# Kernel optimization log

Measured on AMD Instinct MI355X. Metric: run time of the kernel, lower is better.

## Reference

```python
import jax, jax.numpy as jnp
from jax import lax
import numpy as np

B, W, M, F = 8, 20, 512, 16
H = 128          # n_hidden
HALF = 64        # half_hid
K = 10           # conv out channels
LONG_K = W // 2  # dilated conv kernel


def setup_inputs() -> dict:
    key = jax.random.key(0)
    ks = jax.random.split(key, 24)
    s = 0.1  # weight scale (xavier-ish)
    return {
        "X": jax.random.normal(ks[0], (B, W, M, F), jnp.float32),
        "Y": jax.random.uniform(ks[1], (B, M), jnp.float32),
        "adj": jax.random.uniform(ks[2], (M, M), jnp.float32),
        "V": jax.random.normal(ks[3], (HALF,), jnp.float32) * s,
        "bv": jax.random.normal(ks[4], (1,), jnp.float32) * s,
        "W1": jax.random.normal(ks[5], (HALF, H), jnp.float32) * s,
        "b1": jax.random.normal(ks[6], (HALF,), jnp.float32) * s,
        "W2": jax.random.normal(ks[7], (HALF, H), jnp.float32) * s,
        "Wb": jax.random.normal(ks[8], (M, M), jnp.float32) * s,
        "wb": jax.random.normal(ks[9], (1,), jnp.float32) * s,
        "conv_w": jax.random.normal(ks[10], (K, F, W), jnp.float32) * s,
        "conv_b": jax.random.normal(ks[11], (K,), jnp.float32) * s,
        "convl_w": jax.random.normal(ks[12], (K, F, LONG_K), jnp.float32) * s,
        "convl_b": jax.random.normal(ks[13], (K,), jnp.float32) * s,
        "gru_Wih": jax.random.normal(ks[14], (3 * H, F), jnp.float32) * s,
        "gru_Whh": jax.random.normal(ks[15], (3 * H, H), jnp.float32) * s,
        "gru_bih": jax.random.normal(ks[16], (3 * H,), jnp.float32) * s,
        "gru_bhh": jax.random.normal(ks[17], (3 * H,), jnp.float32) * s,
        "gc1_W": jax.random.normal(ks[18], (3 * K, H), jnp.float32) * s,
        "gc1_b": jax.random.normal(ks[19], (H,), jnp.float32) * s,
        "gc2_W": jax.random.normal(ks[20], (H, K), jnp.float32) * s,
        "gc2_b": jax.random.normal(ks[21], (K,), jnp.float32) * s,
        "out_W": jax.random.normal(ks[22], (1, H + K), jnp.float32) * s,
        "out_b": jax.random.normal(ks[23], (1,), jnp.float32) * s,
    }


def _gru_last(xseq, Wih, Whh, bih, bhh):
    # xseq: (N, T, F) -> last hidden (N, H), PyTorch GRU gate order r,z,n
    n_hid = Whh.shape[1]
    def step(h, x_t):
        gx = x_t @ Wih.T + bih
        gh = h @ Whh.T + bhh
        xr, xz, xn = jnp.split(gx, 3, axis=-1)
        hr, hz, hn = jnp.split(gh, 3, axis=-1)
        r = jax.nn.sigmoid(xr + hr)
        z = jax.nn.sigmoid(xz + hz)
        n = jnp.tanh(xn + r * hn)
        return (1.0 - z) * n + z * h, None
    h0 = jnp.zeros((xseq.shape[0], n_hid), xseq.dtype)
    hT, _ = lax.scan(step, h0, jnp.moveaxis(xseq, 1, 0))
    return hT


def _forward(X, Y, adj, V, bv, W1, b1, W2, Wb, wb, conv_w, conv_b, convl_w,
             convl_b, gru_Wih, gru_Whh, gru_bih, gru_bhh, gc1_W, gc1_b,
             gc2_W, gc2_b, out_W, out_b):
    b, w, m, f = X.shape
    # ---- temporal branch: GRU per node ----
    x = jnp.transpose(X, (0, 2, 1, 3)).reshape(b * m, w, f)
    last_hid = _gru_last(x, gru_Wih, gru_Whh, gru_bih, gru_bhh).reshape(b, m, -1)
    out_temporal = last_hid
    # ---- attention-style adaptive adjacency ----
    # hid_rpt_m[b,i,j]=last_hid[b,j]; hid_rpt_w[b,i,j]=last_hid[b,i]
    p1 = jnp.einsum('bjh,kh->bjk', last_hid, W1)  # pairs with column index j
    p2 = jnp.einsum('bih,kh->bik', last_hid, W2)  # pairs with row index i
    pre = p1[:, None, :, :] + p2[:, :, None, :] + b1  # (b,m,m,half)
    a_mx = jnp.einsum('bijk,k->bij', jax.nn.elu(pre), V) + bv[0]
    # F.normalize(p=2, dim=1)
    nrm = jnp.sqrt(jnp.sum(a_mx * a_mx, axis=1, keepdims=True))
    a_mx = a_mx / jnp.maximum(nrm, 1e-12)
    # ---- per-node conv1d (vectorized over nodes) ----
    Xc = jnp.transpose(X, (0, 2, 3, 1)).reshape(b * m, f, w)  # (bm, f, w)
    dn = ('NCH', 'OIH', 'NCH')
    r = lax.conv_general_dilated(Xc, conv_w, (1,), 'VALID', dimension_numbers=dn)
    r = r + conv_b[None, :, None]                      # (bm, K, 1)
    rl = lax.conv_general_dilated(Xc, convl_w, (1,), 'VALID',
                                  rhs_dilation=(2,), dimension_numbers=dn)
    rl = rl + convl_b[None, :, None]                   # (bm, K, long_out)
    r_cat = jnp.concatenate([r, rl], axis=-1)          # (bm, K, 1+long_out)
    r_l = jax.nn.relu(r_cat.reshape(b, m, -1))         # (b, m, (1+long_out)*K)
    # ---- gate learned adjacency with fixed adjacency ----
    c = jax.nn.sigmoid(jnp.einsum('bij,jk->bik', a_mx, Wb) + wb[0])
    A = adj[None] * c + a_mx * (1.0 - c)               # (b,m,m)
    # ---- graph convolutions: out = A @ (x @ W) + b ----
    h1 = jax.nn.relu(jnp.einsum('bij,bjh->bih', A, r_l @ gc1_W) + gc1_b)
    out_spatial = jax.nn.relu(jnp.einsum('bij,bjh->bih', A, h1 @ gc2_W) + gc2_b)
    # ---- readout ----
    out = jnp.concatenate([out_spatial, out_temporal], axis=-1)
    out = (out @ out_W.T + out_b).squeeze(-1)          # (b, m)
    y = out.reshape(-1)
    Yf = Y.reshape(-1)
    # BCE with logits: softplus(y) - Y*y, averaged
    loss = jnp.mean(jax.nn.softplus(y) - Yf * y)
    return loss, jax.nn.sigmoid(y)


def reference(X, Y, adj, V, bv, W1, b1, W2, Wb, wb, conv_w, conv_b, convl_w,
              convl_b, gru_Wih, gru_Whh, gru_bih, gru_bhh, gc1_W, gc1_b,
              gc2_W, gc2_b, out_W, out_b):
    return _forward(X, Y, adj, V, bv, W1, b1, W2, Wb, wb, conv_w, conv_b,
                    convl_w, convl_b, gru_Wih, gru_Whh, gru_bih, gru_bhh,
                    gc1_W, gc1_b, gc2_W, gc2_b, out_W, out_b)
```

## Files before the change

### kernel.cpp

```cpp
#include <hip/hip_runtime.h>
#include <math.h>

#define Bn 8
#define Wn 20
#define Mn 512
#define Fn 16
#define Hn 128
#define HALFn 64
#define Kn 10

typedef __attribute__((ext_vector_type(8))) short short8;
typedef __attribute__((ext_vector_type(4))) float f32x4;
typedef unsigned short ushort_t;

__device__ __forceinline__ float sigmoidf_(float x) {
  return 1.0f / (1.0f + __expf(-x));
}
__device__ __forceinline__ float tanhf_(float x) {
  float xx = fminf(fmaxf(x, -15.f), 15.f);
  float e = __expf(2.f * xx);
  return (e - 1.f) / (e + 1.f);
}
__device__ __forceinline__ float reluf_(float x) { return fmaxf(x, 0.f); }
__device__ __forceinline__ float eluf_(float x) {
  return (x > 0.f) ? x : (__expf(x) - 1.f);
}
__device__ __forceinline__ ushort_t bf16_rne(float v) {
  unsigned u = __float_as_uint(v);
  u += 0x7FFFu + ((u >> 16) & 1u);
  return (ushort_t)(u >> 16);
}
__device__ __forceinline__ float bf16_to_f(ushort_t b) {
  return __uint_as_float(((unsigned)b) << 16);
}

__global__ __launch_bounds__(256) void pack_kernel(
    const float* __restrict__ Whh, const float* __restrict__ Wih,
    const float* __restrict__ Wb, ushort_t* __restrict__ Bpack,
    ushort_t* __restrict__ WbT_hi, ushort_t* __restrict__ WbT_lo,
    float* __restrict__ ssq, float* __restrict__ d_out) {
  int tid = threadIdx.x;
  if (blockIdx.x < 240) {
    int idx = blockIdx.x * 256 + tid;
    if (idx < 4096) ssq[idx] = 0.f;
    if (idx == 0) d_out[0] = 0.f;
    if (idx >= 24 * 5 * 512) return;
    int j = idx & 7;
    int lane = (idx >> 3) & 63;
    int ks = (idx >> 9) % 5;
    int nt = idx / (5 * 512);
    int k = ks * 32 + (lane >> 4) * 8 + j;
    int g = (nt & 7) * 16 + (nt >> 3) * 128 + (lane & 15);
    float val = 0.f;
    if (k < 128) val = Whh[g * 128 + k];
    else if (k < 144) val = Wih[g * 16 + (k - 128)];
    ushort_t hb = bf16_rne(val);
    float lo = val - bf16_to_f(hb);
    Bpack[(((long)nt * 5 + ks) * 2 + 0) * 512 + lane * 8 + j] = hb;
    Bpack[(((long)nt * 5 + ks) * 2 + 1) * 512 + lane * 8 + j] = bf16_rne(lo);
  } else {
    int t = blockIdx.x - 240;
    int k0 = (t >> 3) * 64, j0 = (t & 7) * 64;
    __shared__ float wt[64][65];
    for (int idx = tid; idx < 4096; idx += 256) {
      int r = idx >> 6, c = idx & 63;
      wt[r][c] = Wb[(long)(k0 + r) * 512 + j0 + c];
    }
    __syncthreads();
    for (int idx = tid; idx < 4096; idx += 256) {
      int r = idx >> 6, c = idx & 63;
      float v = wt[c][r];
      ushort_t hb = bf16_rne(v);
      WbT_hi[(long)(j0 + r) * 512 + k0 + c] = hb;
      WbT_lo[(long)(j0 + r) * 512 + k0 + c] = bf16_rne(v - bf16_to_f(hb));
    }
  }
}

#define LDK 168
#define HSZ (16 * LDK)
__global__ __launch_bounds__(512, 1) void gru_kernel(
    const float* __restrict__ X, const ushort_t* __restrict__ Bpack,
    const float* __restrict__ bih, const float* __restrict__ bhh,
    const float* __restrict__ W1, const float* __restrict__ W2,
    const float* __restrict__ b1, float* __restrict__ last_hid,
    float* __restrict__ p1, float* __restrict__ p2) {
  const int tid = threadIdx.x;
  const int wave = tid >> 6;
  const int lane = tid & 63;
  const int quad = lane >> 4;
  const int jl = lane & 15;
  const int j0 = wave * 16;
  const int blk = blockIdx.x;
  const int b = blk >> 5;
  const int m0 = (blk & 31) * 16;

  __shared__ __align__(16) ushort_t smem_hs[4 * HSZ];

  short8 frR[5][2], frZ[5][2], frN[4][2], frXN[2];
#pragma unroll
  for (int ks = 0; ks < 5; ++ks) {
#pragma unroll
    for (int p = 0; p < 2; ++p) {
      frR[ks][p] = *(const short8*)&Bpack[(((long)(wave) * 5 + ks) * 2 + p) * 512 + lane * 8];
      frZ[ks][p] = *(const short8*)&Bpack[(((long)(8 + wave) * 5 + ks) * 2 + p) * 512 + lane * 8];
    }
  }
#pragma unroll
  for (int ks = 0; ks < 4; ++ks) {
#pragma unroll
    for (int p = 0; p < 2; ++p)
      frN[ks][p] = *(const short8*)&Bpack[(((long)(16 + wave) * 5 + ks) * 2 + p) * 512 + lane * 8];
  }
#pragma unroll
  for (int p = 0; p < 2; ++p)
    frXN[p] = *(const short8*)&Bpack[(((long)(16 + wave) * 5 + 4) * 2 + p) * 512 + lane * 8];

  const float cr  = bih[j0 + jl] + bhh[j0 + jl];
  const float cz  = bih[128 + j0 + jl] + bhh[128 + j0 + jl];
  const float cnx = bih[256 + j0 + jl];
  const float cnh = bhh[256 + j0 + jl];

  for (int i = tid; i < 4 * HSZ; i += 512) smem_hs[i] = 0;

  const float* Xb = X + (long)b * (Wn * Mn * Fn) + (long)m0 * Fn;
  float x0 = 0.f;
  if (tid < 256) x0 = Xb[tid];
// ... 42 lines not shown
#pragma unroll
    for (int reg = 0; reg < 4; ++reg) {
      float r = sigmoidf_(aR[0][reg] + aR[1][reg] + cr);
      float z = sigmoidf_(aZ[0][reg] + aZ[1][reg] + cz);
      float n = tanhf_(aXN[reg] + cnx + r * (aHN[0][reg] + aHN[1][reg] + cnh));
      float h = (1.f - z) * n + z * hp[reg];
      hp[reg] = h;
      int s = quad * 4 + reg;
      ushort_t hb = bf16_rne(h);
      smem_hs[hiN + s * LDK + j0 + jl] = hb;
      smem_hs[loN + s * LDK + j0 + jl] = bf16_rne(h - bf16_to_f(hb));
    }
    if (tid < 256 && t < Wn - 1) {
      int s = tid >> 4, f = tid & 15;
      ushort_t hb = bf16_rne(xpre);
      smem_hs[hiN + s * LDK + 128 + f] = hb;
      smem_hs[loN + s * LDK + 128 + f] = bf16_rne(xpre - bf16_to_f(hb));
    }
    __syncthreads();
  }

  float* hs_f = (float*)smem_hs;
#pragma unroll
  for (int reg = 0; reg < 4; ++reg) {
    int s = quad * 4 + reg;
    float h = hp[reg];
    last_hid[(long)(blk * 16 + s) * Hn + j0 + jl] = h;
    hs_f[s * 132 + j0 + jl] = h;
  }
  __syncthreads();
  {
    int k = tid & 63;
    int part = (tid >> 6) & 1;
    int sg = tid >> 7;
    const float* Wp = part ? W2 : W1;
    float a[4];
    float init = part ? 0.f : b1[k];
    a[0] = a[1] = a[2] = a[3] = init;
    for (int h = 0; h < 128; h += 4) {
      float4 w = *(const float4*)&Wp[k * 128 + h];
#pragma unroll
      for (int rr = 0; rr < 4; ++rr) {
        float4 q = *(const float4*)&hs_f[(sg * 4 + rr) * 132 + h];
        a[rr] += q.x * w.x + q.y * w.y + q.z * w.z + q.w * w.w;
      }
    }
    float* outp = part ? p2 : p1;
#pragma unroll
    for (int rr = 0; rr < 4; ++rr)
      outp[(long)(blk * 16 + sg * 4 + rr) * 64 + k] = a[rr];
  }
}

__global__ __launch_bounds__(128) void conv_t1_kernel(
    const float* __restrict__ X, const float* __restrict__ conv_w,
    const float* __restrict__ conv_b, const float* __restrict__ convl_w,
    const float* __restrict__ convl_b, const float* __restrict__ gc1_W,
    ushort_t* __restrict__ t1T_hi, ushort_t* __restrict__ t1T_lo) {
  int tid = threadIdx.x;
  int n0 = blockIdx.x * 8;
  int b = n0 >> 9, m0 = n0 & 511;
  __shared__ float xs[8][16][20];
  __shared__ float cw[3200];
  __shared__ float clw[1600];
  __shared__ float rs[8][32];
  for (int idx = tid; idx < 3200; idx += 128) cw[idx] = conv_w[idx];
  for (int idx = tid; idx < 1600; idx += 128) clw[idx] = convl_w[idx];
  for (int w = 0; w < 20; ++w)
    xs[tid >> 4][tid & 15][w] = X[((long)(b * 20 + w) * 512 + m0) * 16 + tid];
  __syncthreads();
  if (tid < 80) {
    int s = tid / 10, k = tid % 10;
    float a0 = conv_b[k];
    float l0 = convl_b[k], l1 = convl_b[k];
    for (int f = 0; f < 16; ++f) {
#pragma unroll
      for (int w = 0; w < 20; ++w) a0 = fmaf(xs[s][f][w], cw[k * 320 + f * 20 + w], a0);
#pragma unroll
      for (int q = 0; q < 10; ++q) {
        float wv = clw[k * 160 + f * 10 + q];
        l0 = fmaf(xs[s][f][2 * q], wv, l0);
        l1 = fmaf(xs[s][f][2 * q + 1], wv, l1);
      }
    }
    rs[s][k * 3 + 0] = reluf_(a0);
    rs[s][k * 3 + 1] = reluf_(l0);
    rs[s][k * 3 + 2] = reluf_(l1);
  }
  __syncthreads();
  float w[30];
#pragma unroll
  for (int q = 0; q < 30; ++q) w[q] = gc1_W[q * 128 + tid];
  long base = ((long)b * 128 + tid) * 512 + m0;
#pragma unroll
  for (int s = 0; s < 8; ++s) {
    float a = 0.f;
#pragma unroll
    for (int q = 0; q < 30; ++q) a = fmaf(rs[s][q], w[q], a);
    ushort_t hb = bf16_rne(a);
    t1T_hi[base + s] = hb;
    t1T_lo[base + s] = bf16_rne(a - bf16_to_f(hb));
  }
}

__global__ __launch_bounds__(256) void amx_kernel(
    const float* __restrict__ p1, const float* __restrict__ p2,
    const float* __restrict__ V, const float* __restrict__ bv,
    float* __restrict__ amx, float* __restrict__ ssq) {
  int tid = threadIdx.x;
  int j0 = blockIdx.x * 32, i0 = blockIdx.y * 32, bz = blockIdx.z;
  __shared__ float p1s[32][68];
  __shared__ float p2s[32][68];
  __shared__ float Vs[64];
  __shared__ float cred[16][33];
  if (tid < 64) Vs[tid] = V[tid];
  {
    int rr = tid >> 3, c0 = (tid & 7) * 8;
    *(float4*)&p1s[rr][c0]     = *(const float4*)&p1[(long)(bz * 512 + j0 + rr) * 64 + c0];
    *(float4*)&p1s[rr][c0 + 4] = *(const float4*)&p1[(long)(bz * 512 + j0 + rr) * 64 + c0 + 4];
    *(float4*)&p2s[rr][c0]     = *(const float4*)&p2[(long)(bz * 512 + i0 + rr) * 64 + c0];
    *(float4*)&p2s[rr][c0 + 4] = *(const float4*)&p2[(long)(bz * 512 + i0 + rr) * 64 + c0 + 4];
  }
  __syncthreads();
  int r0 = tid >> 4, c0 = tid & 15;
  float acc[2][2] = {{0.f, 0.f}, {0.f, 0.f}};
  for (int k = 0; k < 64; ++k) {
    float vj0 = p1s[c0][k], vj1 = p1s[c0 + 16][k];
    float vi0 = p2s[r0][k], vi1 = p2s[r0 + 16][k];
    float vk = Vs[k];
    acc[0][0] = fmaf(eluf_(vj0 + vi0), vk, acc[0][0]);
    acc[0][1] = fmaf(eluf_(vj1 + vi0), vk, acc[0][1]);
    acc[1][0] = fmaf(eluf_(vj0 + vi1), vk, acc[1][0]);
    acc[1][1] = fmaf(eluf_(vj1 + vi1), vk, acc[1][1]);
  }
  float bvv = bv[0];
  float s2[2] = {0.f, 0.f};
#pragma unroll
  for (int a = 0; a < 2; ++a)
#pragma unroll
    for (int c = 0; c < 2; ++c) {
      float v = acc[a][c] + bvv;
      amx[((long)(bz * 512 + i0 + r0 + a * 16)) * 512 + j0 + c0 + c * 16] = v;
      s2[c] += v * v;
    }
  cred[r0][c0] = s2[0];
  cred[r0][c0 + 16] = s2[1];
  __syncthreads();
  if (tid < 32) {
    float s = 0.f;
#pragma unroll
    for (int p = 0; p < 16; ++p) s += cred[p][tid];
    atomicAdd(&ssq[bz * 512 + j0 + tid], s);
  }
}

#define CPK 40
__global__ __launch_bounds__(256, 2) void gemm_cA(
    const float* __restrict__ amx, const ushort_t* __restrict__ WbT_hi,
    const ushort_t* __restrict__ WbT_lo, const float* __restrict__ adj,
    const float* __restrict__ wb, const float* __restrict__ ssq,
    float* __restrict__ A) {
  const int bz = blockIdx.z;
  const int i0 = blockIdx.y * 64;
  const int j0 = blockIdx.x * 64;
  const int tid = threadIdx.x;
  const int wave = tid >> 6;
  const int lane = tid & 63;
  const int quad = lane >> 4, jl = lane & 15;
  const int wm = (wave & 1) * 32, wn = (wave >> 1) * 32;

  __shared__ __align__(16) ushort_t Ahi[64][CPK];
  __shared__ __align__(16) ushort_t Alo[64][CPK];
  __shared__ __align__(16) ushort_t Bhi[64][CPK];
  __shared__ __align__(16) ushort_t Blo[64][CPK];
  __shared__ float rs_s[512];

  const float* Abase = amx + (long)bz * 262144;
  const float* sb = ssq + bz * 512;
  for (int i = tid; i < 512; i += 256)
    rs_s[i] = 1.f / fmaxf(sqrtf(sb[i]), 1e-12f);

  f32x4 acc[2][2];
#pragma unroll
  for (int a = 0; a < 2; ++a)
#pragma unroll
    for (int c = 0; c < 2; ++c) acc[a][c] = (f32x4){0.f, 0.f, 0.f, 0.f};

  for (int kk0 = 0; kk0 < 512; kk0 += 32) {
    __syncthreads();
#pragma unroll
    for (int l = 0; l < 2; ++l) {
      int e = l * 1024 + tid * 4;
      int r = e >> 5, kq = e & 31;
      float4 v = *(const float4*)&Abase[(long)(i0 + r) * 512 + kk0 + kq];
      float4 sc = *(const float4*)&rs_s[kk0 + kq];
      float vv[4] = {v.x * sc.x, v.y * sc.y, v.z * sc.z, v.w * sc.w};
#pragma unroll
      for (int q = 0; q < 4; ++q) {
        ushort_t hb = bf16_rne(vv[q]);
        Ahi[r][kq + q] = hb;
        Alo[r][kq + q] = bf16_rne(vv[q] - bf16_to_f(hb));
      }
    }
    {
      int r = tid >> 2, kc = (tid & 3) * 8;
      *(uint4*)&Bhi[r][kc] = *(const uint4*)&WbT_hi[(long)(j0 + r) * 512 + kk0 + kc];
      *(uint4*)&Blo[r][kc] = *(const uint4*)&WbT_lo[(long)(j0 + r) * 512 + kk0 + kc];
    }
    __syncthreads();
    short8 ah[2], al[2], bh[2], bl[2];
#pragma unroll
    for (int tm = 0; tm < 2; ++tm) {
      ah[tm] = *(const short8*)&Ahi[wm + tm * 16 + jl][quad * 8];
      al[tm] = *(const short8*)&Alo[wm + tm * 16 + jl][quad * 8];
    }
#pragma unroll
    for (int tn = 0; tn < 2; ++tn) {
      bh[tn] = *(const short8*)&Bhi[wn + tn * 16 + jl][quad * 8];
      bl[tn] = *(const short8*)&Blo[wn + tn * 16 + jl][quad * 8];
    }
#pragma unroll
    for (int tm = 0; tm < 2; ++tm)
#pragma unroll
      for (int tn = 0; tn < 2; ++tn) {
        acc[tm][tn] = __builtin_amdgcn_mfma_f32_16x16x32_bf16(ah[tm], bh[tn], acc[tm][tn], 0, 0, 0);
        acc[tm][tn] = __builtin_amdgcn_mfma_f32_16x16x32_bf16(ah[tm], bl[tn], acc[tm][tn], 0, 0, 0);
        acc[tm][tn] = __builtin_amdgcn_mfma_f32_16x16x32_bf16(al[tm], bh[tn], acc[tm][tn], 0, 0, 0);
      }
  }

  const float wbv = wb[0];
#pragma unroll
  for (int tn = 0; tn < 2; ++tn) {
    int j = j0 + wn + tn * 16 + jl;
    float sj = rs_s[j];
#pragma unroll
    for (int tm = 0; tm < 2; ++tm) {
#pragma unroll
      for (int reg = 0; reg < 4; ++reg) {
        int i = i0 + wm + tm * 16 + quad * 4 + reg;
        long ofs = (long)bz * 262144 + (long)i * 512 + j;
        float c = sigmoidf_(acc[tm][tn][reg] + wbv);
        float am = Abase[(long)i * 512 + j] * sj;
        float ad = adj[(long)i * 512 + j];
        A[ofs] = ad * c + am * (1.f - c);
      }
    }
  }
}

__global__ __launch_bounds__(512, 1) void gemm_h1t2(
    const float* __restrict__ A, const ushort_t* __restrict__ t1T_hi,
    const ushort_t* __restrict__ t1T_lo, const float* __restrict__ gc1_b,
    const float* __restrict__ gc2_W, float* __restrict__ t2) {
  const int bz = blockIdx.y;
  const int i0 = blockIdx.x * 16;
  const int tid = threadIdx.x;
  const int wave = tid >> 6;
  const int lane = tid & 63;
  const int quad = lane >> 4, jl = lane & 15;

  __shared__ __align__(16) ushort_t Ahi[16][CPK];
  __shared__ __align__(16) ushort_t Alo[16][CPK];
  __shared__ __align__(16) ushort_t Bhi[128][CPK];
  __shared__ __align__(16) ushort_t Blo[128][CPK];
  __shared__ float h1s[16][132];
  __shared__ float gw[1280];

  const float* Ab = A + (long)bz * 262144;
  for (int idx = tid; idx < 1280; idx += 512) gw[idx] = gc2_W[idx];

  f32x4 acc = {0.f, 0.f, 0.f, 0.f};

  for (int kk0 = 0; kk0 < 512; kk0 += 32) {
    __syncthreads();
    {
      int r = tid >> 5, kq = tid & 31;
      float v = Ab[(long)(i0 + r) * 512 + kk0 + kq];
      ushort_t hb = bf16_rne(v);
      Ahi[r][kq] = hb;
      Alo[r][kq] = bf16_rne(v - bf16_to_f(hb));
    }
    {
      int r = tid >> 2, kc = (tid & 3) * 8;
      *(uint4*)&Bhi[r][kc] = *(const uint4*)&t1T_hi[((long)bz * 128 + r) * 512 + kk0 + kc];
      *(uint4*)&Blo[r][kc] = *(const uint4*)&t1T_lo[((long)bz * 128 + r) * 512 + kk0 + kc];
    }
    __syncthreads();
    short8 ah = *(const short8*)&Ahi[jl][quad * 8];
    short8 al = *(const short8*)&Alo[jl][quad * 8];
    short8 bh = *(const short8*)&Bhi[wave * 16 + jl][quad * 8];
    short8 bl = *(const short8*)&Blo[wave * 16 + jl][quad * 8];
    acc = __builtin_amdgcn_mfma_f32_16x16x32_bf16(ah, bh, acc, 0, 0, 0);
    acc = __builtin_amdgcn_mfma_f32_16x16x32_bf16(ah, bl, acc, 0, 0, 0);
    acc = __builtin_amdgcn_mfma_f32_16x16x32_bf16(al, bh, acc, 0, 0, 0);
  }
  __syncthreads();
  {
    int n = wave * 16 + jl;
    float bb = gc1_b[n];
#pragma unroll
    for (int reg = 0; reg < 4; ++reg) {
      int r = quad * 4 + reg;
      h1s[r][n] = reluf_(acc[reg] + bb);
    }
  }
  __syncthreads();
  if (tid < 160) {
    int r = tid / 10, c = tid % 10;
    float a = 0.f;
#pragma unroll 4
    for (int k = 0; k < 128; ++k) a = fmaf(h1s[r][k], gw[k * 10 + c], a);
    t2[((long)bz * 512 + i0 + r) * 10 + c] = a;
  }
}

__global__ __launch_bounds__(256) void spat_readout(
    const float* __restrict__ A, const float* __restrict__ t2,
    const float* __restrict__ gc2_b, const float* __restrict__ last_hid,
    const float* __restrict__ out_W, const float* __restrict__ out_b,
    const float* __restrict__ Y, float* __restrict__ d_out) {
  int tid = threadIdx.x;
  int bz = blockIdx.y;
  int i0 = blockIdx.x * 8;
  __shared__ float t2s[5120];
  __shared__ float wS[138];
  __shared__ float osps[8][12];
  for (int idx = tid; idx < 5120; idx += 256) t2s[idx] = t2[(long)bz * 5120 + idx];
  for (int idx = tid; idx < 138; idx += 256) wS[idx] = out_W[idx];
  __syncthreads();
  int r = tid >> 5, sk = tid & 31;
  const float* Arow = A + (long)bz * 262144 + (long)(i0 + r) * 512;
  float acc[10] = {0, 0, 0, 0, 0, 0, 0, 0, 0, 0};
  for (int k = sk; k < 512; k += 32) {
    float av = Arow[k];
    const float* tp = &t2s[k * 10];
#pragma unroll
    for (int c = 0; c < 10; ++c) acc[c] = fmaf(av, tp[c], acc[c]);
  }
#pragma unroll
  for (int off = 16; off; off >>= 1)
#pragma unroll
    for (int c = 0; c < 10; ++c) acc[c] += __shfl_xor(acc[c], off);
  if (sk == 0) {
#pragma unroll
    for (int c = 0; c < 10; ++c) osps[r][c] = reluf_(acc[c] + gc2_b[c]);
  }
  __syncthreads();
  float l = 0.f;
  if (tid < 8) {
    int gid = bz * 512 + i0 + tid;
    float y = out_b[0];
#pragma unroll
    for (int k = 0; k < 10; ++k) y = fmaf(osps[tid][k], wS[k], y);
    const float* hp = &last_hid[(long)gid * 128];
    for (int h = 0; h < 128; h += 4) {
      float4 hv = *(const float4*)&hp[h];
      y = fmaf(hv.x, wS[10 + h + 0], y);
      y = fmaf(hv.y, wS[10 + h + 1], y);
      y = fmaf(hv.z, wS[10 + h + 2], y);
      y = fmaf(hv.w, wS[10 + h + 3], y);
    }
    d_out[1 + gid] = sigmoidf_(y);
    l = fmaxf(y, 0.f) + log1pf(__expf(-fabsf(y))) - Y[gid] * y;
  }
  if (tid < 64) {
#pragma unroll
    for (int off = 4; off; off >>= 1) l += __shfl_down(l, off);
    if (tid == 0) atomicAdd(d_out, l * (1.0f / 4096.f));
  }
}

extern "C" void kernel_launch(void* const* d_in, const int* in_sizes, int n_in,
                              void* d_out, int out_size, void* d_ws, size_t ws_size,
                              hipStream_t stream) {
  const float* X       = (const float*)d_in[0];
  const float* Y       = (const float*)d_in[1];
  const float* adj     = (const float*)d_in[2];
  const float* V       = (const float*)d_in[3];
  const float* bv      = (const float*)d_in[4];
  const float* W1      = (const float*)d_in[5];
  const float* b1      = (const float*)d_in[6];
  const float* W2      = (const float*)d_in[7];
  const float* Wb      = (const float*)d_in[8];
  const float* wb      = (const float*)d_in[9];
  const float* conv_w  = (const float*)d_in[10];
  const float* conv_b  = (const float*)d_in[11];
  const float* convl_w = (const float*)d_in[12];
  const float* convl_b = (const float*)d_in[13];
  const float* gWih    = (const float*)d_in[14];
  const float* gWhh    = (const float*)d_in[15];
  const float* gbih    = (const float*)d_in[16];
  const float* gbhh    = (const float*)d_in[17];
  const float* gc1_W   = (const float*)d_in[18];
  const float* gc1_b   = (const float*)d_in[19];
  const float* gc2_W   = (const float*)d_in[20];
  const float* gc2_b   = (const float*)d_in[21];
  const float* out_W   = (const float*)d_in[22];
  const float* out_b   = (const float*)d_in[23];
  float* out = (float*)d_out;

  float* ws = (float*)d_ws;
  float* lhid  = ws; ws += 524288;
  float* p1    = ws; ws += 262144;
  float* p2    = ws; ws += 262144;
  float* amx   = ws; ws += 2097152;
  float* ssq   = ws; ws += 4096;
  float* Abuf  = ws; ws += 2097152;
  float* t2    = ws; ws += 40960;
  float* Bpkf  = ws; ws += 122880;
  float* WbTf  = ws; ws += 262144;
  float* t1Tf  = ws; ws += 524288;
  if (ws_size < (size_t)(ws - (float*)d_ws) * sizeof(float)) return;
  ushort_t* Bpack  = (ushort_t*)Bpkf;
  ushort_t* WbT_hi = (ushort_t*)WbTf;
  ushort_t* WbT_lo = WbT_hi + 262144;
  ushort_t* t1T_hi = (ushort_t*)t1Tf;
  ushort_t* t1T_lo = t1T_hi + 524288;

  pack_kernel<<<304, 256, 0, stream>>>(gWhh, gWih, Wb, Bpack, WbT_hi, WbT_lo,
                                       ssq, out);
  gru_kernel<<<256, 512, 0, stream>>>(X, Bpack, gbih, gbhh, W1, W2, b1,
                                      lhid, p1, p2);
  conv_t1_kernel<<<512, 128, 0, stream>>>(X, conv_w, conv_b, convl_w, convl_b,
                                          gc1_W, t1T_hi, t1T_lo);
  amx_kernel<<<dim3(16, 16, 8), 256, 0, stream>>>(p1, p2, V, bv, amx, ssq);
  gemm_cA<<<dim3(8, 8, 8), 256, 0, stream>>>(amx, WbT_hi, WbT_lo, adj, wb,
                                             ssq, Abuf);
  gemm_h1t2<<<dim3(32, 8), 512, 0, stream>>>(Abuf, t1T_hi, t1T_lo, gc1_b,
                                             gc2_W, t2);
  spat_readout<<<dim3(64, 8), 256, 0, stream>>>(Abuf, t2, gc2_b, lhid,
                                                out_W, out_b, Y, out);
}
```

Measured before the change: 256.1 us.

## Fuse pack with conv and merge tail stages into one cooperative kernel

Merges the weight-packing and conv/t1 kernels into one prep kernel, and folds the amx, gate GEMM, graph-conv GEMM and readout kernels into a single cooperative kernel separated by grid-wide syncs. The amx stage now has each block own a column strip, so column norms are computed locally with no atomics and no ssq zeroing. The aim is to remove launch gaps and inter-kernel drain between many small stages. In exchange it adds grid.sync overhead and fixes the tail to 512 blocks of 256 threads, which needs two resident blocks per CU; the h1/t2 stage uses only half the grid.

```diff
diff --git a/kernel.cpp b/kernel.cpp
--- a/kernel.cpp
+++ b/kernel.cpp
@@ -1,13 +1,14 @@
 #include <hip/hip_runtime.h>
+#include <hip/hip_cooperative_groups.h>
 #include <math.h>
+
+namespace cg = cooperative_groups;
 
 #define Bn 8
 #define Wn 20
 #define Mn 512
 #define Fn 16
 #define Hn 128
-#define HALFn 64
-#define Kn 10
 
 typedef __attribute__((ext_vector_type(8))) short short8;
 typedef __attribute__((ext_vector_type(4))) float f32x4;
@@ -34,45 +35,99 @@
   return __uint_as_float(((unsigned)b) << 16);
 }
 
-__global__ __launch_bounds__(256) void pack_kernel(
+__global__ __launch_bounds__(256) void prep_kernel(
+    const float* __restrict__ X, const float* __restrict__ conv_w,
+    const float* __restrict__ conv_b, const float* __restrict__ convl_w,
+    const float* __restrict__ convl_b, const float* __restrict__ gc1_W,
     const float* __restrict__ Whh, const float* __restrict__ Wih,
     const float* __restrict__ Wb, ushort_t* __restrict__ Bpack,
     ushort_t* __restrict__ WbT_hi, ushort_t* __restrict__ WbT_lo,
-    float* __restrict__ ssq, float* __restrict__ d_out) {
-  int tid = threadIdx.x;
-  if (blockIdx.x < 240) {
-    int idx = blockIdx.x * 256 + tid;
-    if (idx < 4096) ssq[idx] = 0.f;
-    if (idx == 0) d_out[0] = 0.f;
-    if (idx >= 24 * 5 * 512) return;
-    int j = idx & 7;
-    int lane = (idx >> 3) & 63;
-    int ks = (idx >> 9) % 5;
-    int nt = idx / (5 * 512);
+    ushort_t* __restrict__ t1T_hi, ushort_t* __restrict__ t1T_lo,
+    float* __restrict__ d_out) {
+  int tid = threadIdx.x, blk = blockIdx.x;
+  __shared__ __align__(16) char sm[30720];
+  float* xs  = (float*)sm;
+  float* cw  = (float*)(sm + 10240);
+  float* clw = (float*)(sm + 23040);
+  float* rs  = (float*)(sm + 29440);
+
+  int gidx = blk * 256 + tid;
+  if (gidx == 0) d_out[0] = 0.f;
+  if (gidx < 24 * 5 * 512) {
+    int j = gidx & 7;
+    int lane = (gidx >> 3) & 63;
+    int ks = (gidx >> 9) % 5;
+    int nt = gidx / (5 * 512);
     int k = ks * 32 + (lane >> 4) * 8 + j;
     int g = (nt & 7) * 16 + (nt >> 3) * 128 + (lane & 15);
     float val = 0.f;
     if (k < 128) val = Whh[g * 128 + k];
     else if (k < 144) val = Wih[g * 16 + (k - 128)];
     ushort_t hb = bf16_rne(val);
-    float lo = val - bf16_to_f(hb);
     Bpack[(((long)nt * 5 + ks) * 2 + 0) * 512 + lane * 8 + j] = hb;
-    Bpack[(((long)nt * 5 + ks) * 2 + 1) * 512 + lane * 8 + j] = bf16_rne(lo);
-  } else {
-    int t = blockIdx.x - 240;
-    int k0 = (t >> 3) * 64, j0 = (t & 7) * 64;
-    __shared__ float wt[64][65];
+    Bpack[(((long)nt * 5 + ks) * 2 + 1) * 512 + lane * 8 + j] =
+        bf16_rne(val - bf16_to_f(hb));
+  }
+
+  int n0 = blk * 8, b = n0 >> 9, m0 = n0 & 511;
+  for (int idx = tid; idx < 3200; idx += 256) cw[idx] = conv_w[idx];
+  for (int idx = tid; idx < 1600; idx += 256) clw[idx] = convl_w[idx];
+  if (tid < 128) {
+    for (int w = 0; w < 20; ++w)
+      xs[tid * 20 + w] = X[((long)(b * 20 + w) * 512 + m0) * 16 + tid];
+  }
+  __syncthreads();
+  if (tid < 80) {
+    int s = tid / 10, k = tid % 10;
+    float a0 = conv_b[k];
+    float l0 = convl_b[k], l1 = convl_b[k];
+    for (int f = 0; f < 16; ++f) {
+      const float* xp = &xs[(s * 16 + f) * 20];
+#pragma unroll
+      for (int w = 0; w < 20; ++w) a0 = fmaf(xp[w], cw[k * 320 + f * 20 + w], a0);
+#pragma unroll
+      for (int q = 0; q < 10; ++q) {
+        float wv = clw[k * 160 + f * 10 + q];
+        l0 = fmaf(xp[2 * q], wv, l0);
+        l1 = fmaf(xp[2 * q + 1], wv, l1);
+      }
+    }
+    rs[s * 32 + k * 3 + 0] = reluf_(a0);
+    rs[s * 32 + k * 3 + 1] = reluf_(l0);
+    rs[s * 32 + k * 3 + 2] = reluf_(l1);
+  }
+  __syncthreads();
+  if (tid < 128) {
+    float w[30];
+#pragma unroll
+    for (int q = 0; q < 30; ++q) w[q] = gc1_W[q * 128 + tid];
+    long base = ((long)b * 128 + tid) * 512 + m0;
+#pragma unroll
+    for (int s = 0; s < 8; ++s) {
+      float a = 0.f;
+#pragma unroll
+      for (int q = 0; q < 30; ++q) a = fmaf(rs[s * 32 + q], w[q], a);
+      ushort_t hb = bf16_rne(a);
+      t1T_hi[base + s] = hb;
+      t1T_lo[base + s] = bf16_rne(a - bf16_to_f(hb));
+    }
+  }
+
+  if (blk < 64) {
+    __syncthreads();
+    float* wt = (float*)sm;
+    int k0 = (blk >> 3) * 64, j0w = (blk & 7) * 64;
     for (int idx = tid; idx < 4096; idx += 256) {
       int r = idx >> 6, c = idx & 63;
-      wt[r][c] = Wb[(long)(k0 + r) * 512 + j0 + c];
+      wt[r * 65 + c] = Wb[(long)(k0 + r) * 512 + j0w + c];
     }
     __syncthreads();
     for (int idx = tid; idx < 4096; idx += 256) {
       int r = idx >> 6, c = idx & 63;
-      float v = wt[c][r];
+      float v = wt[c * 65 + r];
       ushort_t hb = bf16_rne(v);
-      WbT_hi[(long)(j0 + r) * 512 + k0 + c] = hb;
-      WbT_lo[(long)(j0 + r) * 512 + k0 + c] = bf16_rne(v - bf16_to_f(hb));
+      WbT_hi[(long)(j0w + r) * 512 + k0 + c] = hb;
+      WbT_lo[(long)(j0w + r) * 512 + k0 + c] = bf16_rne(v - bf16_to_f(hb));
     }
   }
 }
@@ -221,322 +276,264 @@
   }
 }
 
-__global__ __launch_bounds__(128) void conv_t1_kernel(
-    const float* __restrict__ X, const float* __restrict__ conv_w,
-    const float* __restrict__ conv_b, const float* __restrict__ convl_w,
-    const float* __restrict__ convl_b, const float* __restrict__ gc1_W,
-    ushort_t* __restrict__ t1T_hi, ushort_t* __restrict__ t1T_lo) {
-  int tid = threadIdx.x;
-  int n0 = blockIdx.x * 8;
-  int b = n0 >> 9, m0 = n0 & 511;
-  __shared__ float xs[8][16][20];
-  __shared__ float cw[3200];
-  __shared__ float clw[1600];
-  __shared__ float rs[8][32];
-  for (int idx = tid; idx < 3200; idx += 128) cw[idx] = conv_w[idx];
-  for (int idx = tid; idx < 1600; idx += 128) clw[idx] = convl_w[idx];
-  for (int w = 0; w < 20; ++w)
-    xs[tid >> 4][tid & 15][w] = X[((long)(b * 20 + w) * 512 + m0) * 16 + tid];
-  __syncthreads();
-  if (tid < 80) {
-    int s = tid / 10, k = tid % 10;
-    float a0 = conv_b[k];
-    float l0 = convl_b[k], l1 = convl_b[k];
-    for (int f = 0; f < 16; ++f) {
-#pragma unroll
-      for (int w = 0; w < 20; ++w) a0 = fmaf(xs[s][f][w], cw[k * 320 + f * 20 + w], a0);
-#pragma unroll
-      for (int q = 0; q < 10; ++q) {
-        float wv = clw[k * 160 + f * 10 + q];
-        l0 = fmaf(xs[s][f][2 * q], wv, l0);
-        l1 = fmaf(xs[s][f][2 * q + 1], wv, l1);
-      }
-    }
-    rs[s][k * 3 + 0] = reluf_(a0);
-    rs[s][k * 3 + 1] = reluf_(l0);
-    rs[s][k * 3 + 2] = reluf_(l1);
-  }
-  __syncthreads();
-  float w[30];
-#pragma unroll
-  for (int q = 0; q < 30; ++q) w[q] = gc1_W[q * 128 + tid];
-  long base = ((long)b * 128 + tid) * 512 + m0;
-#pragma unroll
-  for (int s = 0; s < 8; ++s) {
-    float a = 0.f;
-#pragma unroll
-    for (int q = 0; q < 30; ++q) a = fmaf(rs[s][q], w[q], a);
-    ushort_t hb = bf16_rne(a);
-    t1T_hi[base + s] = hb;
-    t1T_lo[base + s] = bf16_rne(a - bf16_to_f(hb));
-  }
-}
-
-__global__ __launch_bounds__(256) void amx_kernel(
-    const float* __restrict__ p1, const float* __restrict__ p2,
-    const float* __restrict__ V, const float* __restrict__ bv,
-    float* __restrict__ amx, float* __restrict__ ssq) {
-  int tid = threadIdx.x;
-  int j0 = blockIdx.x * 32, i0 = blockIdx.y * 32, bz = blockIdx.z;
-  __shared__ float p1s[32][68];
-  __shared__ float p2s[32][68];
-  __shared__ float Vs[64];
-  __shared__ float cred[16][33];
-  if (tid < 64) Vs[tid] = V[tid];
-  {
-    int rr = tid >> 3, c0 = (tid & 7) * 8;
-    *(float4*)&p1s[rr][c0]     = *(const float4*)&p1[(long)(bz * 512 + j0 + rr) * 64 + c0];
-    *(float4*)&p1s[rr][c0 + 4] = *(const float4*)&p1[(long)(bz * 512 + j0 + rr) * 64 + c0 + 4];
-    *(float4*)&p2s[rr][c0]     = *(const float4*)&p2[(long)(bz * 512 + i0 + rr) * 64 + c0];
-    *(float4*)&p2s[rr][c0 + 4] = *(const float4*)&p2[(long)(bz * 512 + i0 + rr) * 64 + c0 + 4];
-  }
-  __syncthreads();
-  int r0 = tid >> 4, c0 = tid & 15;
-  float acc[2][2] = {{0.f, 0.f}, {0.f, 0.f}};
-  for (int k = 0; k < 64; ++k) {
-    float vj0 = p1s[c0][k], vj1 = p1s[c0 + 16][k];
-    float vi0 = p2s[r0][k], vi1 = p2s[r0 + 16][k];
-    float vk = Vs[k];
-    acc[0][0] = fmaf(eluf_(vj0 + vi0), vk, acc[0][0]);
-    acc[0][1] = fmaf(eluf_(vj1 + vi0), vk, acc[0][1]);
-    acc[1][0] = fmaf(eluf_(vj0 + vi1), vk, acc[1][0]);
-    acc[1][1] = fmaf(eluf_(vj1 + vi1), vk, acc[1][1]);
-  }
-  float bvv = bv[0];
-  float s2[2] = {0.f, 0.f};
-#pragma unroll
-  for (int a = 0; a < 2; ++a)
-#pragma unroll
-    for (int c = 0; c < 2; ++c) {
-      float v = acc[a][c] + bvv;
-      amx[((long)(bz * 512 + i0 + r0 + a * 16)) * 512 + j0 + c0 + c * 16] = v;
-      s2[c] += v * v;
-    }
-  cred[r0][c0] = s2[0];
-  cred[r0][c0 + 16] = s2[1];
-  __syncthreads();
-  if (tid < 32) {
-    float s = 0.f;
-#pragma unroll
-    for (int p = 0; p < 16; ++p) s += cred[p][tid];
-    atomicAdd(&ssq[bz * 512 + j0 + tid], s);
-  }
-}
+struct TArgs {
+  const float *p1, *p2, *V, *bv, *adj, *wb, *gc1_b, *gc2_W, *gc2_b;
+  const float *last_hid, *out_W, *out_b, *Y;
+  const ushort_t *WbT_hi, *WbT_lo, *t1T_hi, *t1T_lo;
+  float *amx, *scl, *A, *t2, *out;
+};
 
 #define CPK 40
-__global__ __launch_bounds__(256, 2) void gemm_cA(
-    const float* __restrict__ amx, const ushort_t* __restrict__ WbT_hi,
-    const ushort_t* __restrict__ WbT_lo, const float* __restrict__ adj,
-    const float* __restrict__ wb, const float* __restrict__ ssq,
-    float* __restrict__ A) {
-  const int bz = blockIdx.z;
-  const int i0 = blockIdx.y * 64;
-  const int j0 = blockIdx.x * 64;
+__global__ __launch_bounds__(256, 2) void tail_kernel(TArgs a) {
+  cg::grid_group grid = cg::this_grid();
   const int tid = threadIdx.x;
+  const int blk = blockIdx.x;
   const int wave = tid >> 6;
   const int lane = tid & 63;
   const int quad = lane >> 4, jl = lane & 15;
-  const int wm = (wave & 1) * 32, wn = (wave >> 1) * 32;
-
-  __shared__ __align__(16) ushort_t Ahi[64][CPK];
-  __shared__ __align__(16) ushort_t Alo[64][CPK];
-  __shared__ __align__(16) ushort_t Bhi[64][CPK];
-  __shared__ __align__(16) ushort_t Blo[64][CPK];
-  __shared__ float rs_s[512];
-
-  const float* Abase = amx + (long)bz * 262144;
-  const float* sb = ssq + bz * 512;
-  for (int i = tid; i < 512; i += 256)
-    rs_s[i] = 1.f / fmaxf(sqrtf(sb[i]), 1e-12f);
-
-  f32x4 acc[2][2];
-#pragma unroll
-  for (int a = 0; a < 2; ++a)
-#pragma unroll
-    for (int c = 0; c < 2; ++c) acc[a][c] = (f32x4){0.f, 0.f, 0.f, 0.f};
-
-  for (int kk0 = 0; kk0 < 512; kk0 += 32) {
-    __syncthreads();
-#pragma unroll
-    for (int l = 0; l < 2; ++l) {
-      int e = l * 1024 + tid * 4;
-      int r = e >> 5, kq = e & 31;
-      float4 v = *(const float4*)&Abase[(long)(i0 + r) * 512 + kk0 + kq];
-      float4 sc = *(const float4*)&rs_s[kk0 + kq];
-      float vv[4] = {v.x * sc.x, v.y * sc.y, v.z * sc.z, v.w * sc.w};
-#pragma unroll
-      for (int q = 0; q < 4; ++q) {
-        ushort_t hb = bf16_rne(vv[q]);
-        Ahi[r][kq + q] = hb;
-        Alo[r][kq + q] = bf16_rne(vv[q] - bf16_to_f(hb));
-      }
-    }
-    {
-      int r = tid >> 2, kc = (tid & 3) * 8;
-      *(uint4*)&Bhi[r][kc] = *(const uint4*)&WbT_hi[(long)(j0 + r) * 512 + kk0 + kc];
-      *(uint4*)&Blo[r][kc] = *(const uint4*)&WbT_lo[(long)(j0 + r) * 512 + kk0 + kc];
-    }
-    __syncthreads();
-    short8 ah[2], al[2], bh[2], bl[2];
-#pragma unroll
-    for (int tm = 0; tm < 2; ++tm) {
-      ah[tm] = *(const short8*)&Ahi[wm + tm * 16 + jl][quad * 8];
-      al[tm] = *(const short8*)&Alo[wm + tm * 16 + jl][quad * 8];
-    }
+  __shared__ __align__(16) char sm[36864];
+
+  {
+    float* Vs   = (float*)sm;
+    float* p1s  = (float*)(sm + 256);
+    float* p2s  = (float*)(sm + 2432);
+    float* sred = (float*)(sm + 11136);
+    int j0 = (blk & 63) * 8, bz = blk >> 6;
+    if (tid < 64) Vs[tid] = a.V[tid];
+    for (int idx = tid; idx < 512; idx += 256) {
+      int r = idx >> 6, k = idx & 63;
+      p1s[r * 68 + k] = a.p1[(long)(bz * 512 + j0 + r) * 64 + k];
+    }
+    float bvv = a.bv[0];
+    int r = tid >> 3, c = tid & 7;
+    float ss = 0.f;
+    for (int it = 0; it < 16; ++it) {
+      int i0 = it * 32;
+      __syncthreads();
+      for (int idx = tid; idx < 2048; idx += 256) {
+        int rr = idx >> 6, k = idx & 63;
+        p2s[rr * 68 + k] = a.p2[(long)(bz * 512 + i0 + rr) * 64 + k];
+      }
+      __syncthreads();
+      float acc = 0.f;
+#pragma unroll 4
+      for (int k = 0; k < 64; ++k)
+        acc = fmaf(eluf_(p1s[c * 68 + k] + p2s[r * 68 + k]), Vs[k], acc);
+      float v = acc + bvv;
+      a.amx[((long)(bz * 512 + i0 + r)) * 512 + j0 + c] = v;
+      ss += v * v;
+    }
+    sred[r * 8 + c] = ss;
+    __syncthreads();
+    if (tid < 8) {
+      float s = 0.f;
+#pragma unroll
+      for (int p = 0; p < 32; ++p) s += sred[p * 8 + tid];
+      a.scl[bz * 512 + j0 + tid] = 1.f / fmaxf(sqrtf(s), 1e-12f);
+    }
+  }
+  __threadfence();
+  grid.sync();
+
+  {
+    ushort_t* Ahi = (ushort_t*)sm;
+    ushort_t* Alo = (ushort_t*)(sm + 5120);
+    ushort_t* Bhi = (ushort_t*)(sm + 10240);
+    ushort_t* Blo = (ushort_t*)(sm + 15360);
+    float*    rsS = (float*)(sm + 20480);
+    int bx = blk & 7, by = (blk >> 3) & 7, bz = blk >> 6;
+    int i0 = by * 64, j0 = bx * 64;
+    const int wm = (wave & 1) * 32, wn = (wave >> 1) * 32;
+    const float* Abase = a.amx + (long)bz * 262144;
+    for (int i = tid; i < 512; i += 256) rsS[i] = a.scl[bz * 512 + i];
+
+    f32x4 acc[2][2];
+#pragma unroll
+    for (int q = 0; q < 2; ++q)
+#pragma unroll
+      for (int w = 0; w < 2; ++w) acc[q][w] = (f32x4){0.f, 0.f, 0.f, 0.f};
+
+    for (int kk0 = 0; kk0 < 512; kk0 += 32) {
+      __syncthreads();
+#pragma unroll
+      for (int l = 0; l < 2; ++l) {
+        int e = l * 1024 + tid * 4;
+        int r = e >> 5, kq = e & 31;
+        float4 v = *(const float4*)&Abase[(long)(i0 + r) * 512 + kk0 + kq];
+        float4 sc = *(const float4*)&rsS[kk0 + kq];
+        float vv[4] = {v.x * sc.x, v.y * sc.y, v.z * sc.z, v.w * sc.w};
+#pragma unroll
+        for (int q = 0; q < 4; ++q) {
+          ushort_t hb = bf16_rne(vv[q]);
+          Ahi[r * CPK + kq + q] = hb;
+          Alo[r * CPK + kq + q] = bf16_rne(vv[q] - bf16_to_f(hb));
+        }
+      }
+      {
+        int r = tid >> 2, kc = (tid & 3) * 8;
+        *(uint4*)&Bhi[r * CPK + kc] = *(const uint4*)&a.WbT_hi[(long)(j0 + r) * 512 + kk0 + kc];
+        *(uint4*)&Blo[r * CPK + kc] = *(const uint4*)&a.WbT_lo[(long)(j0 + r) * 512 + kk0 + kc];
+      }
+      __syncthreads();
+      short8 ah[2], al[2], bh[2], bl[2];
+#pragma unroll
+      for (int tm = 0; tm < 2; ++tm) {
+        ah[tm] = *(const short8*)&Ahi[(wm + tm * 16 + jl) * CPK + quad * 8];
+        al[tm] = *(const short8*)&Alo[(wm + tm * 16 + jl) * CPK + quad * 8];
+      }
+#pragma unroll
+      for (int tn = 0; tn < 2; ++tn) {
+        bh[tn] = *(const short8*)&Bhi[(wn + tn * 16 + jl) * CPK + quad * 8];
+        bl[tn] = *(const short8*)&Blo[(wn + tn * 16 + jl) * CPK + quad * 8];
+      }
+#pragma unroll
+      for (int tm = 0; tm < 2; ++tm)
+#pragma unroll
+        for (int tn = 0; tn < 2; ++tn) {
+          acc[tm][tn] = __builtin_amdgcn_mfma_f32_16x16x32_bf16(ah[tm], bh[tn], acc[tm][tn], 0, 0, 0);
+          acc[tm][tn] = __builtin_amdgcn_mfma_f32_16x16x32_bf16(ah[tm], bl[tn], acc[tm][tn], 0, 0, 0);
+          acc[tm][tn] = __builtin_amdgcn_mfma_f32_16x16x32_bf16(al[tm], bh[tn], acc[tm][tn], 0, 0, 0);
+        }
+    }
+    const float wbv = a.wb[0];
 #pragma unroll
     for (int tn = 0; tn < 2; ++tn) {
-      bh[tn] = *(const short8*)&Bhi[wn + tn * 16 + jl][quad * 8];
-      bl[tn] = *(const short8*)&Blo[wn + tn * 16 + jl][quad * 8];
-    }
-#pragma unroll
-    for (int tm = 0; tm < 2; ++tm)
+      int j = j0 + wn + tn * 16 + jl;
+      float sj = rsS[j];
+#pragma unroll
+      for (int tm = 0; tm < 2; ++tm) {
+#pragma unroll
+        for (int reg = 0; reg < 4; ++reg) {
+          int i = i0 + wm + tm * 16 + quad * 4 + reg;
+          long ofs = (long)bz * 262144 + (long)i * 512 + j;
+          float c = sigmoidf_(acc[tm][tn][reg] + wbv);
+          float am = Abase[(long)i * 512 + j] * sj;
+          float ad = a.adj[(long)i * 512 + j];
+          a.A[ofs] = ad * c + am * (1.f - c);
+        }
+      }
+    }
+  }
+  __threadfence();
+  grid.sync();
+
+  if (blk < 256) {
+    ushort_t* Ahi = (ushort_t*)sm;
+    ushort_t* Alo = (ushort_t*)(sm + 1280);
+    ushort_t* Bhi = (ushort_t*)(sm + 2560);
+    ushort_t* Blo = (ushort_t*)(sm + 12800);
+    float*    h1s = (float*)(sm + 23040);
+    float*    gw  = (float*)(sm + 31488);
+    int ib = blk & 31, bz = blk >> 5;
+    int i0 = ib * 16;
+    const float* Ab = a.A + (long)bz * 262144;
+    for (int idx = tid; idx < 1280; idx += 256) gw[idx] = a.gc2_W[idx];
+
+    f32x4 acc[2];
+    acc[0] = acc[1] = (f32x4){0.f, 0.f, 0.f, 0.f};
+    for (int kk0 = 0; kk0 < 512; kk0 += 32) {
+      __syncthreads();
+      {
+        int e = tid * 2;
+        int r = e >> 5, kq = e & 31;
+        float2 v = *(const float2*)&Ab[(long)(i0 + r) * 512 + kk0 + kq];
+        ushort_t hb0 = bf16_rne(v.x);
+        Ahi[r * CPK + kq] = hb0;
+        Alo[r * CPK + kq] = bf16_rne(v.x - bf16_to_f(hb0));
+        ushort_t hb1 = bf16_rne(v.y);
+        Ahi[r * CPK + kq + 1] = hb1;
+        Alo[r * CPK + kq + 1] = bf16_rne(v.y - bf16_to_f(hb1));
+      }
+#pragma unroll
+      for (int l = 0; l < 2; ++l) {
+        int e = l * 2048 + tid * 8;
+        int r = e >> 5, kc = e & 31;
+        *(uint4*)&Bhi[r * CPK + kc] = *(const uint4*)&a.t1T_hi[((long)bz * 128 + r) * 512 + kk0 + kc];
+        *(uint4*)&Blo[r * CPK + kc] = *(const uint4*)&a.t1T_lo[((long)bz * 128 + r) * 512 + kk0 + kc];
+      }
+      __syncthreads();
+      short8 ah = *(const short8*)&Ahi[jl * CPK + quad * 8];
+      short8 al = *(const short8*)&Alo[jl * CPK + quad * 8];
 #pragma unroll
       for (int tn = 0; tn < 2; ++tn) {
-        acc[tm][tn] = __builtin_amdgcn_mfma_f32_16x16x32_bf16(ah[tm], bh[tn], acc[tm][tn], 0, 0, 0);
-        acc[tm][tn] = __builtin_amdgcn_mfma_f32_16x16x32_bf16(ah[tm], bl[tn], acc[tm][tn], 0, 0, 0);
-        acc[tm][tn] = __builtin_amdgcn_mfma_f32_16x16x32_bf16(al[tm], bh[tn], acc[tm][tn], 0, 0, 0);
-      }
-  }
-
-  const float wbv = wb[0];
-#pragma unroll
-  for (int tn = 0; tn < 2; ++tn) {
-    int j = j0 + wn + tn * 16 + jl;
-    float sj = rs_s[j];
-#pragma unroll
-    for (int tm = 0; tm < 2; ++tm) {
+        short8 bh = *(const short8*)&Bhi[(wave * 32 + tn * 16 + jl) * CPK + quad * 8];
+        short8 bl = *(const short8*)&Blo[(wave * 32 + tn * 16 + jl) * CPK + quad * 8];
+        acc[tn] = __builtin_amdgcn_mfma_f32_16x16x32_bf16(ah, bh, acc[tn], 0, 0, 0);
+        acc[tn] = __builtin_amdgcn_mfma_f32_16x16x32_bf16(ah, bl, acc[tn], 0, 0, 0);
+        acc[tn] = __builtin_amdgcn_mfma_f32_16x16x32_bf16(al, bh, acc[tn], 0, 0, 0);
+      }
+    }
+    __syncthreads();
+#pragma unroll
+    for (int tn = 0; tn < 2; ++tn) {
+      int n = wave * 32 + tn * 16 + jl;
+      float bb = a.gc1_b[n];
 #pragma unroll
       for (int reg = 0; reg < 4; ++reg) {
-        int i = i0 + wm + tm * 16 + quad * 4 + reg;
-        long ofs = (long)bz * 262144 + (long)i * 512 + j;
-        float c = sigmoidf_(acc[tm][tn][reg] + wbv);
-        float am = Abase[(long)i * 512 + j] * sj;
-        float ad = adj[(long)i * 512 + j];
-        A[ofs] = ad * c + am * (1.f - c);
-      }
-    }
-  }
-}
-
-__global__ __launch_bounds__(512, 1) void gemm_h1t2(
-    const float* __restrict__ A, const ushort_t* __restrict__ t1T_hi,
-    const ushort_t* __restrict__ t1T_lo, const float* __restrict__ gc1_b,
-    const float* __restrict__ gc2_W, float* __restrict__ t2) {
-  const int bz = blockIdx.y;
-  const int i0 = blockIdx.x * 16;
-  const int tid = threadIdx.x;
-  const int wave = tid >> 6;
-  const int lane = tid & 63;
-  const int quad = lane >> 4, jl = lane & 15;
-
-  __shared__ __align__(16) ushort_t Ahi[16][CPK];
-  __shared__ __align__(16) ushort_t Alo[16][CPK];
-  __shared__ __align__(16) ushort_t Bhi[128][CPK];
-  __shared__ __align__(16) ushort_t Blo[128][CPK];
-  __shared__ float h1s[16][132];
-  __shared__ float gw[1280];
-
-  const float* Ab = A + (long)bz * 262144;
-  for (int idx = tid; idx < 1280; idx += 512) gw[idx] = gc2_W[idx];
-
-  f32x4 acc = {0.f, 0.f, 0.f, 0.f};
-
-  for (int kk0 = 0; kk0 < 512; kk0 += 32) {
-    __syncthreads();
-    {
-      int r = tid >> 5, kq = tid & 31;
-      float v = Ab[(long)(i0 + r) * 512 + kk0 + kq];
-      ushort_t hb = bf16_rne(v);
-      Ahi[r][kq] = hb;
-      Alo[r][kq] = bf16_rne(v - bf16_to_f(hb));
-    }
-    {
-      int r = tid >> 2, kc = (tid & 3) * 8;
-      *(uint4*)&Bhi[r][kc] = *(const uint4*)&t1T_hi[((long)bz * 128 + r) * 512 + kk0 + kc];
-      *(uint4*)&Blo[r][kc] = *(const uint4*)&t1T_lo[((long)bz * 128 + r) * 512 + kk0 + kc];
-    }
-    __syncthreads();
-    short8 ah = *(const short8*)&Ahi[jl][quad * 8];
-    short8 al = *(const short8*)&Alo[jl][quad * 8];
-    short8 bh = *(const short8*)&Bhi[wave * 16 + jl][quad * 8];
-    short8 bl = *(const short8*)&Blo[wave * 16 + jl][quad * 8];
-    acc = __builtin_amdgcn_mfma_f32_16x16x32_bf16(ah, bh, acc, 0, 0, 0);
-    acc = __builtin_amdgcn_mfma_f32_16x16x32_bf16(ah, bl, acc, 0, 0, 0);
-    acc = __builtin_amdgcn_mfma_f32_16x16x32_bf16(al, bh, acc, 0, 0, 0);
-  }
-  __syncthreads();
+        int r = quad * 4 + reg;
+        h1s[r * 132 + n] = reluf_(acc[tn][reg] + bb);
+      }
+    }
+    __syncthreads();
+    if (tid < 160) {
+      int r = tid / 10, c = tid % 10;
+      float s = 0.f;
+#pragma unroll 4
+      for (int k = 0; k < 128; ++k) s = fmaf(h1s[r * 132 + k], gw[k * 10 + c], s);
+      a.t2[((long)bz * 512 + i0 + r) * 10 + c] = s;
+    }
+  }
+  __threadfence();
+  grid.sync();
+
   {
-    int n = wave * 16 + jl;
-    float bb = gc1_b[n];
-#pragma unroll
-    for (int reg = 0; reg < 4; ++reg) {
-      int r = quad * 4 + reg;
-      h1s[r][n] = reluf_(acc[reg] + bb);
-    }
-  }
-  __syncthreads();
-  if (tid < 160) {
-    int r = tid / 10, c = tid % 10;
-    float a = 0.f;
-#pragma unroll 4
-    for (int k = 0; k < 128; ++k) a = fmaf(h1s[r][k], gw[k * 10 + c], a);
-    t2[((long)bz * 512 + i0 + r) * 10 + c] = a;
-  }
-}
-
-__global__ __launch_bounds__(256) void spat_readout(
-    const float* __restrict__ A, const float* __restrict__ t2,
-    const float* __restrict__ gc2_b, const float* __restrict__ last_hid,
-    const float* __restrict__ out_W, const float* __restrict__ out_b,
-    const float* __restrict__ Y, float* __restrict__ d_out) {
-  int tid = threadIdx.x;
-  int bz = blockIdx.y;
-  int i0 = blockIdx.x * 8;
-  __shared__ float t2s[5120];
-  __shared__ float wS[138];
-  __shared__ float osps[8][12];
-  for (int idx = tid; idx < 5120; idx += 256) t2s[idx] = t2[(long)bz * 5120 + idx];
-  for (int idx = tid; idx < 138; idx += 256) wS[idx] = out_W[idx];
-  __syncthreads();
-  int r = tid >> 5, sk = tid & 31;
-  const float* Arow = A + (long)bz * 262144 + (long)(i0 + r) * 512;
-  float acc[10] = {0, 0, 0, 0, 0, 0, 0, 0, 0, 0};
-  for (int k = sk; k < 512; k += 32) {
-    float av = Arow[k];
-    const float* tp = &t2s[k * 10];
-#pragma unroll
-    for (int c = 0; c < 10; ++c) acc[c] = fmaf(av, tp[c], acc[c]);
-  }
-#pragma unroll
-  for (int off = 16; off; off >>= 1)
-#pragma unroll
-    for (int c = 0; c < 10; ++c) acc[c] += __shfl_xor(acc[c], off);
-  if (sk == 0) {
-#pragma unroll
-    for (int c = 0; c < 10; ++c) osps[r][c] = reluf_(acc[c] + gc2_b[c]);
-  }
-  __syncthreads();
-  float l = 0.f;
-  if (tid < 8) {
-    int gid = bz * 512 + i0 + tid;
-    float y = out_b[0];
-#pragma unroll
-    for (int k = 0; k < 10; ++k) y = fmaf(osps[tid][k], wS[k], y);
-    const float* hp = &last_hid[(long)gid * 128];
-    for (int h = 0; h < 128; h += 4) {
-      float4 hv = *(const float4*)&hp[h];
-      y = fmaf(hv.x, wS[10 + h + 0], y);
-      y = fmaf(hv.y, wS[10 + h + 1], y);
-      y = fmaf(hv.z, wS[10 + h + 2], y);
-      y = fmaf(hv.w, wS[10 + h + 3], y);
-    }
-    d_out[1 + gid] = sigmoidf_(y);
-    l = fmaxf(y, 0.f) + log1pf(__expf(-fabsf(y))) - Y[gid] * y;
-  }
-  if (tid < 64) {
-#pragma unroll
-    for (int off = 4; off; off >>= 1) l += __shfl_down(l, off);
-    if (tid == 0) atomicAdd(d_out, l * (1.0f / 4096.f));
+    float* t2s  = (float*)sm;
+    float* wS   = (float*)(sm + 20480);
+    float* osps = (float*)(sm + 21056);
+    int i0 = (blk & 63) * 8, bz = blk >> 6;
+    for (int idx = tid; idx < 5120; idx += 256) t2s[idx] = a.t2[(long)bz * 5120 + idx];
+    for (int idx = tid; idx < 138; idx += 256) wS[idx] = a.out_W[idx];
+    __syncthreads();
+    int r = tid >> 5, sk = tid & 31;
+    const float* Arow = a.A + (long)bz * 262144 + (long)(i0 + r) * 512;
+    float acc[10] = {0, 0, 0, 0, 0, 0, 0, 0, 0, 0};
+    for (int k = sk; k < 512; k += 32) {
+      float av = Arow[k];
+      const float* tp = &t2s[k * 10];
+#pragma unroll
+      for (int c = 0; c < 10; ++c) acc[c] = fmaf(av, tp[c], acc[c]);
+    }
+#pragma unroll
+    for (int off = 16; off; off >>= 1)
+#pragma unroll
+      for (int c = 0; c < 10; ++c) acc[c] += __shfl_xor(acc[c], off);
+    if (sk == 0) {
+#pragma unroll
+      for (int c = 0; c < 10; ++c) osps[r * 12 + c] = reluf_(acc[c] + a.gc2_b[c]);
+    }
+    __syncthreads();
+    float l = 0.f;
+    if (tid < 8) {
+      int gid = bz * 512 + i0 + tid;
+      float y = a.out_b[0];
+#pragma unroll
+      for (int k = 0; k < 10; ++k) y = fmaf(osps[tid * 12 + k], wS[k], y);
+      const float* hp = &a.last_hid[(long)gid * 128];
+      for (int h = 0; h < 128; h += 4) {
+        float4 hv = *(const float4*)&hp[h];
+        y = fmaf(hv.x, wS[10 + h + 0], y);
+        y = fmaf(hv.y, wS[10 + h + 1], y);
+        y = fmaf(hv.z, wS[10 + h + 2], y);
+        y = fmaf(hv.w, wS[10 + h + 3], y);
+      }
+      a.out[1 + gid] = sigmoidf_(y);
+      l = fmaxf(y, 0.f) + log1pf(__expf(-fabsf(y))) - a.Y[gid] * y;
+    }
+    if (tid < 64) {
+#pragma unroll
+      for (int off = 4; off; off >>= 1) l += __shfl_down(l, off);
+      if (tid == 0) atomicAdd(a.out, l * (1.0f / 4096.f));
+    }
   }
 }
 
@@ -574,7 +571,7 @@
   float* p1    = ws; ws += 262144;
   float* p2    = ws; ws += 262144;
   float* amx   = ws; ws += 2097152;
-  float* ssq   = ws; ws += 4096;
+  float* scl   = ws; ws += 4096;
   float* Abuf  = ws; ws += 2097152;
   float* t2    = ws; ws += 40960;
   float* Bpkf  = ws; ws += 122880;
@@ -587,17 +584,19 @@
   ushort_t* t1T_hi = (ushort_t*)t1Tf;
   ushort_t* t1T_lo = t1T_hi + 524288;
 
-  pack_kernel<<<304, 256, 0, stream>>>(gWhh, gWih, Wb, Bpack, WbT_hi, WbT_lo,
-                                       ssq, out);
+  prep_kernel<<<512, 256, 0, stream>>>(X, conv_w, conv_b, convl_w, convl_b,
+                                       gc1_W, gWhh, gWih, Wb, Bpack,
+                                       WbT_hi, WbT_lo, t1T_hi, t1T_lo, out);
   gru_kernel<<<256, 512, 0, stream>>>(X, Bpack, gbih, gbhh, W1, W2, b1,
                                       lhid, p1, p2);
-  conv_t1_kernel<<<512, 128, 0, stream>>>(X, conv_w, conv_b, convl_w, convl_b,
-                                          gc1_W, t1T_hi, t1T_lo);
-  amx_kernel<<<dim3(16, 16, 8), 256, 0, stream>>>(p1, p2, V, bv, amx, ssq);
-  gemm_cA<<<dim3(8, 8, 8), 256, 0, stream>>>(amx, WbT_hi, WbT_lo, adj, wb,
-                                             ssq, Abuf);
-  gemm_h1t2<<<dim3(32, 8), 512, 0, stream>>>(Abuf, t1T_hi, t1T_lo, gc1_b,
-                                             gc2_W, t2);
-  spat_readout<<<dim3(64, 8), 256, 0, stream>>>(Abuf, t2, gc2_b, lhid,
-                                                out_W, out_b, Y, out);
-}
+
+  TArgs ta;
+  ta.p1 = p1; ta.p2 = p2; ta.V = V; ta.bv = bv; ta.adj = adj; ta.wb = wb;
+  ta.gc1_b = gc1_b; ta.gc2_W = gc2_W; ta.gc2_b = gc2_b;
+  ta.last_hid = lhid; ta.out_W = out_W; ta.out_b = out_b; ta.Y = Y;
+  ta.WbT_hi = WbT_hi; ta.WbT_lo = WbT_lo; ta.t1T_hi = t1T_hi; ta.t1T_lo = t1T_lo;
+  ta.amx = amx; ta.scl = scl; ta.A = Abuf; ta.t2 = t2; ta.out = out;
+  void* kargs[] = {(void*)&ta};
+  hipLaunchCooperativeKernel((const void*)tail_kernel, dim3(512), dim3(256),
+                             kargs, 0, stream);
+}
```

Measured after the change: 603.8 us. +135.8%, slower.
